# Optimization experiments

Measured on AMD Instinct MI355X. Metric: run time of the kernel, lower is better.

The kernel has to match this reference:

```python
import jax, jax.numpy as jnp
import numpy as np

NUM_HEADS = 16


def setup_inputs() -> dict:
    key = jax.random.key(0)
    ks = jax.random.split(key, 8)
    B, S, E = 2, 2048, 1024
    std = 0.02
    return {
        "q": jax.random.normal(ks[0], (B, S, E), dtype=jnp.float32),
        "k": jax.random.normal(ks[1], (B, S, E), dtype=jnp.float32),
        "v": jax.random.normal(ks[2], (B, S, E), dtype=jnp.float32),
        "Wq": jax.random.normal(ks[3], (E, E), dtype=jnp.float32) * std,
        "Wk": jax.random.normal(ks[4], (E, E), dtype=jnp.float32) * std,
        "Wv": jax.random.normal(ks[5], (E, E), dtype=jnp.float32) * std,
        "Wo": jax.random.normal(ks[6], (E, E), dtype=jnp.float32) * std,
        "bo": jnp.zeros((E,), dtype=jnp.float32),
    }


def reference(q, k, v, Wq, Wk, Wv, Wo, bo):
    B, S, E = q.shape
    H = NUM_HEADS
    D = E // H
    # projections (nn.Linear: x @ W.T)
    Q = (q @ Wq.T).reshape(B, S, H, D).transpose(0, 2, 1, 3)  # [B,H,S,D]
    K = (k @ Wk.T).reshape(B, S, H, D).transpose(0, 2, 1, 3)
    V = (v @ Wv.T).reshape(B, S, H, D).transpose(0, 2, 1, 3)
    scores = jnp.einsum("bhsd,bhtd->bhst", Q, K)  # [B,H,S,S]
    # causal mask applied before scaling (as in source; -inf/sqrt(d) == -inf)
    causal = jnp.tril(jnp.ones((S, S), dtype=bool))
    scores = jnp.where(causal, scores, -jnp.inf)
    scores = scores / np.sqrt(D).astype(np.float32)
    attn = jax.nn.softmax(scores, axis=-1)
    out = jnp.einsum("bhst,bhtd->bhsd", attn, V)  # [B,H,S,D]
    out = out.transpose(0, 2, 1, 3).reshape(B, S, E)
    return out @ Wo.T + bo
```

## Files before the change

### kernel.cpp

```cpp
#include <hip/hip_runtime.h>

typedef unsigned short u16;
typedef __bf16 bf16x8 __attribute__((ext_vector_type(8)));
typedef float f32x4 __attribute__((ext_vector_type(4)));
typedef unsigned u32x4 __attribute__((ext_vector_type(4)));

#define B_ 2
#define S_ 2048
#define E_ 1024
#define H_ 16
#define D_ 64
#define M_ (B_ * S_)

__device__ inline u16 f2bf(float f) {
  union { float f; unsigned int u; } c; c.f = f;
  unsigned int u = c.u;
  return (u16)((u + 0x7FFFu + ((u >> 16) & 1u)) >> 16);
}

__device__ inline f32x4 mfma16(bf16x8 a, bf16x8 b, f32x4 c) {
  return __builtin_amdgcn_mfma_f32_16x16x32_bf16(a, b, c, 0, 0, 0);
}

__device__ inline void gload16(const void* g, void* lds) {
  __builtin_amdgcn_global_load_lds(
      (const __attribute__((address_space(1))) unsigned int*)g,
      (__attribute__((address_space(3))) unsigned int*)lds, 16, 0, 0);
}

struct CvtArgs {
  const float* src[4];
  u16* dst[4];
  int n[4];
};

__global__ __launch_bounds__(256) void cvt_kernel(CvtArgs a) {
  const int arr = blockIdx.y;
  const int n = a.n[arr];
  const float* __restrict__ s = a.src[arr];
  u16* __restrict__ d = a.dst[arr];
  const int stride = gridDim.x * blockDim.x;
  for (int i = blockIdx.x * blockDim.x + threadIdx.x; i * 4 < n; i += stride) {
    const float4 f = *(const float4*)(s + 4 * i);
    ushort4 o;
    o.x = f2bf(f.x); o.y = f2bf(f.y); o.z = f2bf(f.z); o.w = f2bf(f.w);
    *(ushort4*)(d + 4 * i) = o;
  }
}

__global__ __launch_bounds__(256, 3) void qkv_gemm(
    const float* __restrict__ qf, const float* __restrict__ kf,
    const float* __restrict__ vf, const u16* __restrict__ Wqb,
    const u16* __restrict__ Wkb, const u16* __restrict__ Wvb,
    u16* __restrict__ Qh, u16* __restrict__ Kh, u16* __restrict__ Vt) {
  constexpr int BM = 128, BN = 128, BK = 32;
  __shared__ alignas(16) u16 As[3][BM * BK];
  __shared__ alignas(16) u16 Bs[3][BN * BK];

  const int wg = blockIdx.x;
  const int xcd = wg & 7, idx = wg >> 3;
  const int nb = idx & 7, mz = idx >> 3;
  const int z = mz >> 2;
  const int m0 = (xcd * 4 + (mz & 3)) * BM, n0 = nb * BN;

  const float* A = (z == 0) ? qf  : (z == 1) ? kf  : vf;
  const u16* Bt  = (z == 0) ? Wqb : (z == 1) ? Wkb : Wvb;
  u16* outp      = (z == 0) ? Qh  : (z == 1) ? Kh  : Vt;

  const int tid = threadIdx.x;
  const int wave = tid >> 6, lane = tid & 63;
  const int wm = (wave >> 1) * 64, wn = (wave & 1) * 64;
  const int fr = lane & 15, fc = lane >> 4;
  const int lrow = lane >> 2;
  const int lcol_sw = (((lane & 3) ^ ((lrow >> 1) & 3)) * 8);

  const int arow_sub = lane >> 3;
  const int acol = (lane & 7) * 4;
  const int a_chunkbase = wave * 2;

  f32x4 acc[4][4] = {};

  u16 *aA = As[0], *aB = As[1], *aC = As[2];
  u16 *bA = Bs[0], *bB = Bs[1], *bC = Bs[2];

  float4 areg0[4], areg1[4];

  auto loadA0 = [&](int k0) {
#pragma unroll
    for (int ci = 0; ci < 2; ++ci)
#pragma unroll
      for (int i2 = 0; i2 < 2; ++i2) {
        const int row = (a_chunkbase + ci) * 16 + i2 * 8 + arow_sub;
        areg0[ci * 2 + i2] = *(const float4*)(A + (size_t)(m0 + row) * E_ + k0 + acol);
      }
  };
  auto loadA1 = [&](int k0) {
#pragma unroll
    for (int ci = 0; ci < 2; ++ci)
#pragma unroll
      for (int i2 = 0; i2 < 2; ++i2) {
        const int row = (a_chunkbase + ci) * 16 + i2 * 8 + arow_sub;
        areg1[ci * 2 + i2] = *(const float4*)(A + (size_t)(m0 + row) * E_ + k0 + acol);
      }
  };
  auto writeA0 = [&](u16* as) {
#pragma unroll
    for (int ci = 0; ci < 2; ++ci)
#pragma unroll
      for (int i2 = 0; i2 < 2; ++i2) {
        const int rowLoc = i2 * 8 + arow_sub;
        const int row = (a_chunkbase + ci) * 16 + rowLoc;
        const float4 f = areg0[ci * 2 + i2];
        unsigned d0, d1;
        asm("v_cvt_pk_bf16_f32 %0, %1, %2" : "=v"(d0) : "v"(f.x), "v"(f.y));
        asm("v_cvt_pk_bf16_f32 %0, %1, %2" : "=v"(d1) : "v"(f.z), "v"(f.w));
        const int slot = (acol >> 3) ^ ((rowLoc >> 1) & 3);
        const int half = (acol >> 2) & 1;
        *(uint2*)(&as[row * 32 + slot * 8 + half * 4]) = make_uint2(d0, d1);
      }
  };
  auto writeA1 = [&](u16* as) {
#pragma unroll
    for (int ci = 0; ci < 2; ++ci)
#pragma unroll
      for (int i2 = 0; i2 < 2; ++i2) {
        const int rowLoc = i2 * 8 + arow_sub;
        const int row = (a_chunkbase + ci) * 16 + rowLoc;
        const float4 f = areg1[ci * 2 + i2];
        unsigned d0, d1;
        asm("v_cvt_pk_bf16_f32 %0, %1, %2" : "=v"(d0) : "v"(f.x), "v"(f.y));
        asm("v_cvt_pk_bf16_f32 %0, %1, %2" : "=v"(d1) : "v"(f.z), "v"(f.w));
        const int slot = (acol >> 3) ^ ((rowLoc >> 1) & 3);
        const int half = (acol >> 2) & 1;
        *(uint2*)(&as[row * 32 + slot * 8 + half * 4]) = make_uint2(d0, d1);
      }
  };
  auto loadB = [&](int k0, u16* bs) {
#pragma unroll
    for (int i = 0; i < 2; ++i) {
      const int chunk = wave * 2 + i;
      const int row = chunk * 16 + lrow;
      gload16(Bt + (size_t)(n0 + row) * E_ + k0 + lcol_sw, bs + chunk * 16 * BK);
    }
  };

  const int sl = (fc ^ ((fr >> 1) & 3)) * 8;

  auto compute = [&]() {
    bf16x8 af[4], bfr[4];
#pragma unroll
    for (int mi = 0; mi < 4; ++mi)
      af[mi] = *(const bf16x8*)&aA[(wm + mi * 16 + fr) * BK + sl];
#pragma unroll
    for (int ni = 0; ni < 4; ++ni)
      bfr[ni] = *(const bf16x8*)&bA[(wn + ni * 16 + fr) * BK + sl];
    __builtin_amdgcn_s_setprio(1);
#pragma unroll
    for (int mi = 0; mi < 4; ++mi)
#pragma unroll
      for (int ni = 0; ni < 4; ++ni)
        acc[mi][ni] = mfma16(af[mi], bfr[ni], acc[mi][ni]);
    __builtin_amdgcn_s_setprio(0);
    u16* tp;
    tp = aA; aA = aB; aB = aC; aC = tp;
    tp = bA; bA = bB; bB = bC; bC = tp;
  };

  constexpr int NK = E_ / BK;
  loadA0(0);
  asm volatile("s_waitcnt vmcnt(0)" ::: "memory");
  writeA0(aA);
  loadA1(1 * BK);  loadB(0, bA);
  loadA0(2 * BK);  loadB(1 * BK, bB);

  for (int tt = 0; tt < NK; tt += 2) {
    {
      const int t = tt;
      if (t + 3 < NK) {
        asm volatile("s_waitcnt vmcnt(6)" ::: "memory");
      } else {
        asm volatile("s_waitcnt vmcnt(0)" ::: "memory");
      }
      asm volatile("s_waitcnt lgkmcnt(0)" ::: "memory");
      __builtin_amdgcn_s_barrier();
      __builtin_amdgcn_sched_barrier(0);
      writeA1(aB);
      if (t + 3 < NK) loadA1((t + 3) * BK);
      if (t + 2 < NK) loadB((t + 2) * BK, bC);
      __builtin_amdgcn_sched_barrier(0);
      compute();
    }
    {
      const int t = tt + 1;
      if (t + 1 < NK) {
        if (t + 3 < NK) {
          asm volatile("s_waitcnt vmcnt(6)" ::: "memory");
        } else {
          asm volatile("s_waitcnt vmcnt(0)" ::: "memory");
        }
      } else {
        asm volatile("s_waitcnt vmcnt(0)" ::: "memory");
      }
      asm volatile("s_waitcnt lgkmcnt(0)" ::: "memory");
      __builtin_amdgcn_s_barrier();
      __builtin_amdgcn_sched_barrier(0);
      if (t + 1 < NK) writeA0(aB);
      if (t + 3 < NK) loadA0((t + 3) * BK);
      if (t + 2 < NK) loadB((t + 2) * BK, bC);
      __builtin_amdgcn_sched_barrier(0);
      compute();
    }
  }

#pragma unroll
  for (int mi = 0; mi < 4; ++mi)
#pragma unroll
    for (int ni = 0; ni < 4; ++ni)
#pragma unroll
      for (int r = 0; r < 4; ++r) {
        const int m = m0 + wm + mi * 16 + (fc << 2) + r;
        const int n = n0 + wn + ni * 16 + fr;
        const float v = acc[mi][ni][r];
        const int b = m >> 11, s = m & (S_ - 1), h = n >> 6, d = n & 63;
        if (z != 2) {
          outp[((((size_t)b * H_ + h) * S_ + s) << 6) + d] = f2bf(v);
        } else {
          outp[(((size_t)b * H_ + h) * D_ + d) * S_ + s] = f2bf(v);
        }
      }
}

__global__ __launch_bounds__(256, 4) void oproj_gemm(
    const u16* __restrict__ A, const u16* __restrict__ Bt,
    const float* __restrict__ bias, float* __restrict__ outp) {
  constexpr int BM = 64, BN = 128, BK = 32;
  __shared__ alignas(16) u16 As[3][BM * BK];
  __shared__ alignas(16) u16 Bs[3][BN * BK];

  const int wg = blockIdx.x;
  const int xcd = wg & 7, idx = wg >> 3;
  const int nb = idx & 7, mi_ = idx >> 3;
  const int m0 = (xcd * 8 + mi_) * BM, n0 = nb * BN;

  const int tid = threadIdx.x;
  const int wave = tid >> 6, lane = tid & 63;
  const int wm = (wave >> 1) * 32, wn = (wave & 1) * 64;
  const int fr = lane & 15, fc = lane >> 4;
  const int lrow = lane >> 2;
  const int lcol_sw = (((lane & 3) ^ ((lrow >> 1) & 3)) * 8);

  f32x4 acc[2][4] = {};

  u16 *aA = As[0], *aB = As[1], *aC = As[2];
  u16 *bA = Bs[0], *bB = Bs[1], *bC = Bs[2];

  auto stage = [&](int k0, u16* as, u16* bs) {
#pragma unroll
    for (int i = 0; i < 3; ++i) {
      const int c = wave + 4 * i;
      if (c < 4)
        gload16(A + (size_t)(m0 + c * 16 + lrow) * E_ + k0 + lcol_sw, as + c * 16 * BK);
      else
        gload16(Bt + (size_t)(n0 + (c - 4) * 16 + lrow) * E_ + k0 + lcol_sw,
                bs + (c - 4) * 16 * BK);
    }
  };

  constexpr int NK = E_ / BK;
  stage(0, aA, bA);
  stage(BK, aB, bB);

  const int sl = (fc ^ ((fr >> 1) & 3)) * 8;

  for (int t = 0; t < NK; ++t) {
    if (t + 1 < NK) {
      asm volatile("s_waitcnt vmcnt(3)" ::: "memory");
    } else {
      asm volatile("s_waitcnt vmcnt(0)" ::: "memory");
    }
    __builtin_amdgcn_s_barrier();
    __builtin_amdgcn_sched_barrier(0);

    if (t + 2 < NK) stage((t + 2) * BK, aC, bC);

    bf16x8 af[2], bfr[4];
#pragma unroll
    for (int mi = 0; mi < 2; ++mi)
      af[mi] = *(const bf16x8*)&aA[(wm + mi * 16 + fr) * BK + sl];
#pragma unroll
    for (int ni = 0; ni < 4; ++ni)
      bfr[ni] = *(const bf16x8*)&bA[(wn + ni * 16 + fr) * BK + sl];
    __builtin_amdgcn_s_setprio(1);
#pragma unroll
    for (int mi = 0; mi < 2; ++mi)
#pragma unroll
      for (int ni = 0; ni < 4; ++ni)
        acc[mi][ni] = mfma16(af[mi], bfr[ni], acc[mi][ni]);
    __builtin_amdgcn_s_setprio(0);

    u16* tp;
    tp = aA; aA = aB; aB = aC; aC = tp;
    tp = bA; bA = bB; bB = bC; bC = tp;
  }

#pragma unroll
  for (int mi = 0; mi < 2; ++mi)
#pragma unroll
    for (int ni = 0; ni < 4; ++ni)
#pragma unroll
      for (int r = 0; r < 4; ++r) {
        const int m = m0 + wm + mi * 16 + (fc << 2) + r;
        const int n = n0 + wn + ni * 16 + fr;
        outp[(size_t)m * E_ + n] = acc[mi][ni][r] + bias[n];
      }
}

__device__ __forceinline__ void stage_kv8(
    const u16* __restrict__ Kh_head, const u16* __restrict__ Vt_head,
    int kv0, u16* kb, u16* vb, int wq, int lane) {
  gload16(Kh_head + (size_t)(kv0 + lane) * D_ + wq * 8, kb + wq * 512);
  gload16(Vt_head + (size_t)lane * S_ + kv0 + wq * 8, vb + wq * 512);
}

__global__ __launch_bounds__(512, 4) void flash_attn(
    const u16* __restrict__ Qh, const u16* __restrict__ Kh,
    const u16* __restrict__ Vt, u16* __restrict__ O) {
  __shared__ alignas(16) u16 Kb[3][4096];
  __shared__ alignas(16) u16 Vb[3][4096];

  const int i = blockIdx.x;
  const int ch = i >> 8, p = i & 255;
  const int j = (ch << 8) + ((ch & 1) ? (255 - p) : p);
  const int qt = 15 - (j >> 5);
  const int bh = j & 31;

  const int tid = threadIdx.x;
  const int wq = tid >> 6, lane = tid & 63;

  const int q0 = qt * 128;
  const int b = bh >> 4, h = bh & 15;
  constexpr float SC = 0.125f * 1.4426950408889634f;
  const int fr = lane & 15, fc = lane >> 4;

  const u16* Qbase = Qh + ((size_t)bh * S_ + q0 + wq * 16 + fr) * D_ + 8 * fc;
  const bf16x8 qf0 = *(const bf16x8*)Qbase;
  const bf16x8 qf1 = *(const bf16x8*)(Qbase + 32);
  const u16* Kh_head = Kh + (size_t)bh * S_ * D_;
  const u16* Vt_head = Vt + (size_t)bh * D_ * S_;

  float lacc = 0.f;
  f32x4 oacc[4] = {};
  const int nt = 2 * qt + 2;

  u16 *kA = Kb[0], *kB = Kb[1], *kC = Kb[2];
  u16 *vA = Vb[0], *vB = Vb[1], *vC = Vb[2];

  stage_kv8(Kh_head, Vt_head, 0, kA, vA, wq, lane);
  stage_kv8(Kh_head, Vt_head, 64, kB, vB, wq, lane);

  for (int t = 0; t < nt; ++t) {
    if (t + 1 < nt) {
      asm volatile("s_waitcnt vmcnt(2)" ::: "memory");
    } else {
      asm volatile("s_waitcnt vmcnt(0)" ::: "memory");
    }
    __builtin_amdgcn_s_barrier();
    __builtin_amdgcn_sched_barrier(0);

    if (t + 2 < nt)
      stage_kv8(Kh_head, Vt_head, (t + 2) * 64, kC, vC, wq, lane);

    const u16* kb = kA;
    const u16* vb = vA;

    f32x4 sacc[4] = {};
    __builtin_amdgcn_s_setprio(1);
#pragma unroll
    for (int ni = 0; ni < 4; ++ni) {
      const bf16x8 k0 = *(const bf16x8*)&kb[fc * 512 + (16 * ni + fr) * 8];
      const bf16x8 k1 = *(const bf16x8*)&kb[(fc + 4) * 512 + (16 * ni + fr) * 8];
      sacc[ni] = mfma16(k0, qf0, sacc[ni]);
      sacc[ni] = mfma16(k1, qf1, sacc[ni]);
    }
    __builtin_amdgcn_s_setprio(0);

    const bool diag = (t >= nt - 2);
    const int qg = q0 + wq * 16 + fr;
    const int kvb = t * 64;
#pragma unroll
    for (int ni = 0; ni < 4; ++ni)
#pragma unroll
      for (int r = 0; r < 4; ++r) {
        const int kvg = kvb + 16 * ni + 4 * fc + r;
        float pv;
        if (diag && kvg > qg) {
          pv = 0.f;
        } else {
          pv = __builtin_amdgcn_exp2f(sacc[ni][r] * SC);
        }
        sacc[ni][r] = pv;
        lacc += pv;
      }

    unsigned w[4][2];
#pragma unroll
    for (int ni = 0; ni < 4; ++ni) {
      asm("v_cvt_pk_bf16_f32 %0, %1, %2"
          : "=v"(w[ni][0]) : "v"(sacc[ni][0]), "v"(sacc[ni][1]));
      asm("v_cvt_pk_bf16_f32 %0, %1, %2"
          : "=v"(w[ni][1]) : "v"(sacc[ni][2]), "v"(sacc[ni][3]));
    }

    unsigned paw0[4], paw1[4];
#pragma unroll
    for (int pair = 0; pair < 2; ++pair) {
      unsigned xx[2], yy[2], tt2[2];
#pragma unroll
      for (int hh = 0; hh < 2; ++hh) {
        unsigned a = w[2 * pair][hh], bb = w[2 * pair + 1][hh];
        asm volatile("v_permlane32_swap_b32 %0, %1" : "+v"(a), "+v"(bb));
        xx[hh] = a; yy[hh] = bb;
        const unsigned s = (fc & 1) ? a : bb;
        tt2[hh] = (unsigned)__shfl_xor((int)s, 16);
      }
      unsigned* pw_ = pair ? paw1 : paw0;
      pw_[0] = (fc & 1) ? tt2[0] : xx[0];
      pw_[1] = (fc & 1) ? tt2[1] : xx[1];
      pw_[2] = (fc & 1) ? yy[0] : tt2[0];
      pw_[3] = (fc & 1) ? yy[1] : tt2[1];
    }
    bf16x8 pa0, pa1;
    {
      u32x4 t0 = {paw0[0], paw0[1], paw0[2], paw0[3]};
      u32x4 t1 = {paw1[0], paw1[1], paw1[2], paw1[3]};
      __builtin_memcpy(&pa0, &t0, 16);
      __builtin_memcpy(&pa1, &t1, 16);
    }

    __builtin_amdgcn_s_setprio(1);
#pragma unroll
    for (int nd = 0; nd < 4; ++nd) {
      const bf16x8 v0 = *(const bf16x8*)&vb[fc * 512 + (16 * nd + fr) * 8];
      const bf16x8 v1 = *(const bf16x8*)&vb[(fc + 4) * 512 + (16 * nd + fr) * 8];
      oacc[nd] = mfma16(pa0, v0, oacc[nd]);
      oacc[nd] = mfma16(pa1, v1, oacc[nd]);
    }
    __builtin_amdgcn_s_setprio(0);

    u16* tk = kA; kA = kB; kB = kC; kC = tk;
    u16* tv = vA; vA = vB; vB = vC; vC = tv;
  }

  float l = lacc;
  l += __shfl_xor(l, 16);
  l += __shfl_xor(l, 32);
  float linv[4];
#pragma unroll
  for (int r = 0; r < 4; ++r)
    linv[r] = __builtin_amdgcn_rcpf(__shfl(l, 4 * fc + r));

#pragma unroll
  for (int nd = 0; nd < 4; ++nd) {
#pragma unroll
    for (int r = 0; r < 4; ++r) {
      const int qr = q0 + wq * 16 + (fc << 2) + r;
      const int d = 16 * nd + fr;
      const float v = oacc[nd][r] * linv[r];
      O[((size_t)b * S_ + qr) * E_ + h * D_ + d] = f2bf(v);
    }
  }
}

extern "C" void kernel_launch(void* const* d_in, const int* in_sizes, int n_in,
                              void* d_out, int out_size, void* d_ws, size_t ws_size,
                              hipStream_t stream) {
  const float* q  = (const float*)d_in[0];
  const float* k  = (const float*)d_in[1];
  const float* v  = (const float*)d_in[2];
  const float* Wq = (const float*)d_in[3];
  const float* Wk = (const float*)d_in[4];
  const float* Wv = (const float*)d_in[5];
  const float* Wo = (const float*)d_in[6];
  const float* bo = (const float*)d_in[7];

  const size_t nBSE = (size_t)M_ * E_;
  const size_t nEE  = (size_t)E_ * E_;
  u16* Wqb = (u16*)d_ws;
  u16* Wkb = Wqb + nEE;
  u16* Wvb = Wkb + nEE;
  u16* Wob = Wvb + nEE;
  u16* Qh  = Wob + nEE;
  u16* Kh  = Qh + nBSE;
  u16* Vt  = Kh + nBSE;
  u16* Oa  = Vt + nBSE;

  CvtArgs ca;
  ca.src[0] = Wq; ca.dst[0] = Wqb; ca.n[0] = (int)nEE;
  ca.src[1] = Wk; ca.dst[1] = Wkb; ca.n[1] = (int)nEE;
  ca.src[2] = Wv; ca.dst[2] = Wvb; ca.n[2] = (int)nEE;
  ca.src[3] = Wo; ca.dst[3] = Wob; ca.n[3] = (int)nEE;
  cvt_kernel<<<dim3(256, 4), 256, 0, stream>>>(ca);

  qkv_gemm<<<dim3(768), 256, 0, stream>>>(
      q, k, v, Wqb, Wkb, Wvb, Qh, Kh, Vt);
  flash_attn<<<dim3(512), 512, 0, stream>>>(Qh, Kh, Vt, Oa);
  oproj_gemm<<<dim3(512), 256, 0, stream>>>(Oa, Wob, bo, (float*)d_out);
}
```

Measured before the change: 108.5 us.

## Switch flash attention to 128-wide KV tiles with double buffering

Each loop iteration now stages and processes 128 KV rows instead of 64, moving from a 3-stage ring of 64-row buffers to a 2-stage double buffer of 128-row buffers. The number of barriers and waitcnt synchronisations per block is halved, and each iteration runs two 64-row sub-steps. In exchange, prefetch depth drops to one tile ahead with a full vmcnt(0) wait each iteration, and LDS use rises from 48KB to 64KB per block. That may reduce occupancy and expose more load latency.

Result: faster. 103.1 us (-5.0%).

```diff
diff --git a/kernel.cpp b/kernel.cpp
--- a/kernel.cpp
+++ b/kernel.cpp
@@ -315,18 +315,26 @@
       }
 }
 
-__device__ __forceinline__ void stage_kv8(
+
+__device__ __forceinline__ void stage_kv128(
     const u16* __restrict__ Kh_head, const u16* __restrict__ Vt_head,
     int kv0, u16* kb, u16* vb, int wq, int lane) {
-  gload16(Kh_head + (size_t)(kv0 + lane) * D_ + wq * 8, kb + wq * 512);
-  gload16(Vt_head + (size_t)lane * S_ + kv0 + wq * 8, vb + wq * 512);
+#pragma unroll
+  for (int hh = 0; hh < 2; ++hh)
+    gload16(Kh_head + (size_t)(kv0 + hh * 64 + lane) * D_ + wq * 8,
+            kb + wq * 1024 + hh * 512);
+#pragma unroll
+  for (int i = 0; i < 2; ++i) {
+    const int c = 2 * wq + i;
+    gload16(Vt_head + (size_t)lane * S_ + kv0 + c * 8, vb + c * 512);
+  }
 }
 
 __global__ __launch_bounds__(512, 4) void flash_attn(
     const u16* __restrict__ Qh, const u16* __restrict__ Kh,
     const u16* __restrict__ Vt, u16* __restrict__ O) {
-  __shared__ alignas(16) u16 Kb[3][4096];
-  __shared__ alignas(16) u16 Vb[3][4096];
+  __shared__ alignas(16) u16 Kb[2][8192];
+  __shared__ alignas(16) u16 Vb[2][8192];
 
   const int i = blockIdx.x;
   const int ch = i >> 8, p = i & 255;
@@ -350,105 +358,104 @@
 
   float lacc = 0.f;
   f32x4 oacc[4] = {};
-  const int nt = 2 * qt + 2;
-
-  u16 *kA = Kb[0], *kB = Kb[1], *kC = Kb[2];
-  u16 *vA = Vb[0], *vB = Vb[1], *vC = Vb[2];
-
-  stage_kv8(Kh_head, Vt_head, 0, kA, vA, wq, lane);
-  stage_kv8(Kh_head, Vt_head, 64, kB, vB, wq, lane);
+  const int nt = qt + 1;
+
+  u16 *kA = Kb[0], *kB = Kb[1];
+  u16 *vA = Vb[0], *vB = Vb[1];
+
+  stage_kv128(Kh_head, Vt_head, 0, kA, vA, wq, lane);
 
   for (int t = 0; t < nt; ++t) {
-    if (t + 1 < nt) {
-      asm volatile("s_waitcnt vmcnt(2)" ::: "memory");
-    } else {
-      asm volatile("s_waitcnt vmcnt(0)" ::: "memory");
-    }
+    asm volatile("s_waitcnt vmcnt(0)" ::: "memory");
     __builtin_amdgcn_s_barrier();
     __builtin_amdgcn_sched_barrier(0);
 
-    if (t + 2 < nt)
-      stage_kv8(Kh_head, Vt_head, (t + 2) * 64, kC, vC, wq, lane);
+    if (t + 1 < nt)
+      stage_kv128(Kh_head, Vt_head, (t + 1) * 128, kB, vB, wq, lane);
 
     const u16* kb = kA;
     const u16* vb = vA;
-
-    f32x4 sacc[4] = {};
-    __builtin_amdgcn_s_setprio(1);
-#pragma unroll
-    for (int ni = 0; ni < 4; ++ni) {
-      const bf16x8 k0 = *(const bf16x8*)&kb[fc * 512 + (16 * ni + fr) * 8];
-      const bf16x8 k1 = *(const bf16x8*)&kb[(fc + 4) * 512 + (16 * ni + fr) * 8];
-      sacc[ni] = mfma16(k0, qf0, sacc[ni]);
-      sacc[ni] = mfma16(k1, qf1, sacc[ni]);
-    }
-    __builtin_amdgcn_s_setprio(0);
-
-    const bool diag = (t >= nt - 2);
+    const bool diag = (t == nt - 1);
     const int qg = q0 + wq * 16 + fr;
-    const int kvb = t * 64;
-#pragma unroll
-    for (int ni = 0; ni < 4; ++ni)
-#pragma unroll
-      for (int r = 0; r < 4; ++r) {
-        const int kvg = kvb + 16 * ni + 4 * fc + r;
-        float pv;
-        if (diag && kvg > qg) {
-          pv = 0.f;
-        } else {
-          pv = __builtin_amdgcn_exp2f(sacc[ni][r] * SC);
+
+#pragma unroll
+    for (int hh = 0; hh < 2; ++hh) {
+      const int kvb = t * 128 + hh * 64;
+
+      f32x4 sacc[4] = {};
+      __builtin_amdgcn_s_setprio(1);
+#pragma unroll
+      for (int ni = 0; ni < 4; ++ni) {
+        const bf16x8 k0 = *(const bf16x8*)&kb[fc * 1024 + hh * 512 + (16 * ni + fr) * 8];
+        const bf16x8 k1 = *(const bf16x8*)&kb[(fc + 4) * 1024 + hh * 512 + (16 * ni + fr) * 8];
+        sacc[ni] = mfma16(k0, qf0, sacc[ni]);
+        sacc[ni] = mfma16(k1, qf1, sacc[ni]);
+      }
+      __builtin_amdgcn_s_setprio(0);
+
+#pragma unroll
+      for (int ni = 0; ni < 4; ++ni)
+#pragma unroll
+        for (int r = 0; r < 4; ++r) {
+          const int kvg = kvb + 16 * ni + 4 * fc + r;
+          float pv;
+          if (diag && kvg > qg) {
+            pv = 0.f;
+          } else {
+            pv = __builtin_amdgcn_exp2f(sacc[ni][r] * SC);
+          }
+          sacc[ni][r] = pv;
+          lacc += pv;
         }
-        sacc[ni][r] = pv;
-        lacc += pv;
-      }
-
-    unsigned w[4][2];
-#pragma unroll
-    for (int ni = 0; ni < 4; ++ni) {
-      asm("v_cvt_pk_bf16_f32 %0, %1, %2"
-          : "=v"(w[ni][0]) : "v"(sacc[ni][0]), "v"(sacc[ni][1]));
-      asm("v_cvt_pk_bf16_f32 %0, %1, %2"
-          : "=v"(w[ni][1]) : "v"(sacc[ni][2]), "v"(sacc[ni][3]));
-    }
-
-    unsigned paw0[4], paw1[4];
-#pragma unroll
-    for (int pair = 0; pair < 2; ++pair) {
-      unsigned xx[2], yy[2], tt2[2];
-#pragma unroll
-      for (int hh = 0; hh < 2; ++hh) {
-        unsigned a = w[2 * pair][hh], bb = w[2 * pair + 1][hh];
-        asm volatile("v_permlane32_swap_b32 %0, %1" : "+v"(a), "+v"(bb));
-        xx[hh] = a; yy[hh] = bb;
-        const unsigned s = (fc & 1) ? a : bb;
-        tt2[hh] = (unsigned)__shfl_xor((int)s, 16);
-      }
-      unsigned* pw_ = pair ? paw1 : paw0;
-      pw_[0] = (fc & 1) ? tt2[0] : xx[0];
-      pw_[1] = (fc & 1) ? tt2[1] : xx[1];
-      pw_[2] = (fc & 1) ? yy[0] : tt2[0];
-      pw_[3] = (fc & 1) ? yy[1] : tt2[1];
-    }
-    bf16x8 pa0, pa1;
-    {
-      u32x4 t0 = {paw0[0], paw0[1], paw0[2], paw0[3]};
-      u32x4 t1 = {paw1[0], paw1[1], paw1[2], paw1[3]};
-      __builtin_memcpy(&pa0, &t0, 16);
-      __builtin_memcpy(&pa1, &t1, 16);
-    }
-
-    __builtin_amdgcn_s_setprio(1);
-#pragma unroll
-    for (int nd = 0; nd < 4; ++nd) {
-      const bf16x8 v0 = *(const bf16x8*)&vb[fc * 512 + (16 * nd + fr) * 8];
-      const bf16x8 v1 = *(const bf16x8*)&vb[(fc + 4) * 512 + (16 * nd + fr) * 8];
-      oacc[nd] = mfma16(pa0, v0, oacc[nd]);
-      oacc[nd] = mfma16(pa1, v1, oacc[nd]);
-    }
-    __builtin_amdgcn_s_setprio(0);
-
-    u16* tk = kA; kA = kB; kB = kC; kC = tk;
-    u16* tv = vA; vA = vB; vB = vC; vC = tv;
+
+      unsigned w[4][2];
+#pragma unroll
+      for (int ni = 0; ni < 4; ++ni) {
+        asm("v_cvt_pk_bf16_f32 %0, %1, %2"
+            : "=v"(w[ni][0]) : "v"(sacc[ni][0]), "v"(sacc[ni][1]));
+        asm("v_cvt_pk_bf16_f32 %0, %1, %2"
+            : "=v"(w[ni][1]) : "v"(sacc[ni][2]), "v"(sacc[ni][3]));
+      }
+
+      unsigned paw0[4], paw1[4];
+#pragma unroll
+      for (int pair = 0; pair < 2; ++pair) {
+        unsigned xx[2], yy[2], tt2[2];
+#pragma unroll
+        for (int hh2 = 0; hh2 < 2; ++hh2) {
+          unsigned a = w[2 * pair][hh2], bb = w[2 * pair + 1][hh2];
+          asm volatile("v_permlane32_swap_b32 %0, %1" : "+v"(a), "+v"(bb));
+          xx[hh2] = a; yy[hh2] = bb;
+          const unsigned s = (fc & 1) ? a : bb;
+          tt2[hh2] = (unsigned)__shfl_xor((int)s, 16);
+        }
+        unsigned* pw_ = pair ? paw1 : paw0;
+        pw_[0] = (fc & 1) ? tt2[0] : xx[0];
+        pw_[1] = (fc & 1) ? tt2[1] : xx[1];
+        pw_[2] = (fc & 1) ? yy[0] : tt2[0];
+        pw_[3] = (fc & 1) ? yy[1] : tt2[1];
+      }
+      bf16x8 pa0, pa1;
+      {
+        u32x4 t0 = {paw0[0], paw0[1], paw0[2], paw0[3]};
+        u32x4 t1 = {paw1[0], paw1[1], paw1[2], paw1[3]};
+        __builtin_memcpy(&pa0, &t0, 16);
+        __builtin_memcpy(&pa1, &t1, 16);
+      }
+
+      __builtin_amdgcn_s_setprio(1);
+#pragma unroll
+      for (int nd = 0; nd < 4; ++nd) {
+        const bf16x8 v0 = *(const bf16x8*)&vb[(hh * 8 + fc) * 512 + (16 * nd + fr) * 8];
+        const bf16x8 v1 = *(const bf16x8*)&vb[(hh * 8 + fc + 4) * 512 + (16 * nd + fr) * 8];
+        oacc[nd] = mfma16(pa0, v0, oacc[nd]);
+        oacc[nd] = mfma16(pa1, v1, oacc[nd]);
+      }
+      __builtin_amdgcn_s_setprio(0);
+    }
+
+    u16* tk = kA; kA = kB; kB = tk;
+    u16* tv = vA; vA = vB; vB = tv;
   }
 
   float l = lacc;
```
